# Performance work log

Hardware: AMD Instinct MI355X
Metric: run time of the kernel (lower is better)

Reference implementation:

```python
import jax, jax.numpy as jnp
import numpy as np

C_IN, C_OUT, K, H = 64, 128, 27, 100000

def setup_inputs() -> dict:
    key = jax.random.key(0)
    k1, k2, k3 = jax.random.split(key, 3)
    data_in = jax.random.normal(k1, (1, C_IN, H, 1), dtype=jnp.float32)
    # neighbor index table: 27 neighbors per node; -1 would mean 'missing' (zero-padded)
    neigh = jax.random.randint(k2, (H, K), 0, H, dtype=jnp.int64)
    # conv weight, fan-in scaled init, stored [C_out, C_in, K]
    weight = jax.random.normal(k3, (C_OUT, C_IN, K), dtype=jnp.float32) / np.sqrt(C_IN * K)
    return {"data_in": data_in, "neigh": neigh, "weight": weight}

def reference(data_in, neigh, weight):
    # data_in: [1, C_in, H, 1] (ocnn layout) -> [C_in, H]
    x = data_in[0, :, :, 0]
    # octree2col: gather 27 neighbors per node -> [C_in, H, K]
    cols = x[:, neigh]
    # zero out missing neighbors (index < 0)
    cols = jnp.where(neigh[None, :, :] >= 0, cols, jnp.zeros((), dtype=cols.dtype))
    # GEMM over (C_in, K) fused with ReLU -> [C_out, H]
    out = jnp.einsum('chk,ock->oh', cols, weight)
    out = jax.nn.relu(out)
    return out[None, :, :, None]  # back to ocnn layout [1, C_out, H, 1]
```

## Files before the change

### kernel.cpp

```cpp
#include <hip/hip_runtime.h>
#include <hip/hip_bf16.h>

#define C_IN  64
#define C_OUT 128
#define KK    27
#define HH    100000
#define TB    1563
#define WB    108
#define NBLK  391

typedef __attribute__((ext_vector_type(8))) short s8v;
typedef __attribute__((ext_vector_type(4))) float f32x4;
typedef __attribute__((ext_vector_type(4))) float f4v;
typedef __attribute__((ext_vector_type(4))) int   i4v;

__device__ inline unsigned short f2bf(float f) {
    __hip_bfloat16 h = __float2bfloat16(f);
    return *reinterpret_cast<unsigned short*>(&h);
}

__device__ inline void dma16(const void* g, void* l) {
    __builtin_amdgcn_global_load_lds((const __attribute__((address_space(1))) void*)g,
                                     (__attribute__((address_space(3))) void*)l, 16, 0, 0);
}

__global__ __launch_bounds__(256) void prep_kernel(const float* __restrict__ x,
                                                   const float* __restrict__ w,
                                                   unsigned short* __restrict__ xt,
                                                   unsigned short* __restrict__ wk) {
    const int tid = threadIdx.x;
    if (blockIdx.x < TB) {
        __shared__ __align__(16) unsigned short ts[64 * 72];
        const int hbase = blockIdx.x * 64;
        #pragma unroll
        for (int it = 0; it < 4; ++it) {
            int t = it * 256 + tid;
            int c = t >> 4, hg4 = t & 15;
            int hg = hbase + hg4 * 4;
            f4v v = (f4v){0.f, 0.f, 0.f, 0.f};
            if (hg < HH)
                v = __builtin_nontemporal_load((const f4v*)&x[(size_t)c * HH + hg]);
            ts[(hg4 * 4 + 0) * 72 + c] = f2bf(v.x);
            ts[(hg4 * 4 + 1) * 72 + c] = f2bf(v.y);
            ts[(hg4 * 4 + 2) * 72 + c] = f2bf(v.z);
            ts[(hg4 * 4 + 3) * 72 + c] = f2bf(v.w);
        }
        __syncthreads();
        #pragma unroll
        for (int it = 0; it < 2; ++it) {
            int u = it * 256 + tid;
            int hl = u >> 3, part = u & 7;
            int hg = hbase + hl;
            if (hg < HH)
                __builtin_nontemporal_store(*(const i4v*)&ts[hl * 72 + part * 8],
                                            (i4v*)&xt[(size_t)hg * 64 + part * 8]);
        }
    } else {
        int b = blockIdx.x - TB;
        if (b == 0 && tid < 64) {
            i4v z = (i4v){0, 0, 0, 0};
            *(i4v*)&xt[(size_t)HH * 64 + tid * 8] = z;
        }
        int base = b * 2048 + tid;
        #pragma unroll
        for (int j = 0; j < 8; ++j) {
            int t = base + j * 256;
            int jj = t & 63, o = (t >> 6) & 127, kx = t >> 13;
            int lc = (jj >> 3) ^ (o & 7);
            int c  = lc * 8 + (jj & 7);
            wk[t] = f2bf(w[(size_t)o * (C_IN * KK) + c * KK + kx]);
        }
    }
}

__global__ __launch_bounds__(256, 2) void conv_main(const unsigned short* __restrict__ xt,
                                                    const unsigned short* __restrict__ wk,
                                                    const int* __restrict__ neigh,
                                                    float* __restrict__ out) {
    __shared__ int neigh_s[256 * KK];
    __shared__ __align__(16) unsigned short w_s[2][128 * 64];

    const int tid  = threadIdx.x;
    const int wave = tid >> 6;
    const int lane = tid & 63;
    const int col  = lane & 15;
    const int quad = lane >> 4;
    const int hbase = blockIdx.x * 256;

    #pragma unroll
    for (int i = 0; i < 4; ++i) {
        int row_base = wave * 8 + i * 32;
        dma16(wk + row_base * 64 + lane * 8, &w_s[0][row_base * 64]);
    }

    int4 b0[2][4], b1[2][4];
    {
        #pragma unroll
        for (int nt = 0; nt < 4; ++nt) {
            int n  = wave * 64 + nt * 16 + col;
            int hg = hbase + n;
            int idx = (hg < HH) ? neigh[(size_t)hg * KK] : -1;
            int idxc = (idx < 0) ? HH : idx;
            const unsigned short* base = xt + (size_t)idxc * 64 + quad * 8;
            b0[0][nt] = *(const int4*)(base);
            b0[1][nt] = *(const int4*)(base + 32);
        }
    }

    #pragma unroll
    for (int j = 0; j < KK; ++j) {
        int i = j * 256 + tid;
        int hl = i / KK, kx = i - hl * KK;
        int hg = hbase + hl;
        neigh_s[i] = (hg < HH) ? __builtin_nontemporal_load(&neigh[(size_t)hg * KK + kx]) : -1;
    }

    f32x4 acc[8][4];
    #pragma unroll
    for (int mt = 0; mt < 8; ++mt)
        #pragma unroll
        for (int nt = 0; nt < 4; ++nt)
            acc[mt][nt] = (f32x4){0.f, 0.f, 0.f, 0.f};

    __syncthreads();

    auto loadB = [&](int kk, int4 (&frag)[2][4]) {
        #pragma unroll
        for (int nt = 0; nt < 4; ++nt) {
            int n = wave * 64 + nt * 16 + col;
            int idx = neigh_s[n * KK + kk];
            int idxc = (idx < 0) ? HH : idx;
            const unsigned short* base = xt + (size_t)idxc * 64 + quad * 8;
            frag[0][nt] = *(const int4*)(base);
            frag[1][nt] = *(const int4*)(base + 32);
        }
    };

    auto step = [&](int k, int4 (&cur)[2][4], int4 (&nxt)[2][4], bool last) {
        if (!last) {
            const unsigned short* src = wk + (size_t)(k + 1) * (C_OUT * C_IN);
            unsigned short* dst = &w_s[(k + 1) & 1][0];
            #pragma unroll
            for (int i = 0; i < 4; ++i) {
                int row_base = wave * 8 + i * 32;
                dma16(src + row_base * 64 + lane * 8, dst + row_base * 64);
            }
            loadB(k + 1, nxt);
        }

        const unsigned short* wp = &w_s[k & 1][0];
        #pragma unroll
        for (int ch = 0; ch < 2; ++ch) {
            const int pc = (ch * 4 + quad) ^ (col & 7);
            #pragma unroll
            for (int mt = 0; mt < 8; ++mt) {
                s8v a = *(const s8v*)&wp[(mt * 16 + col) * 64 + pc * 8];
                #pragma unroll
                for (int nt = 0; nt < 4; ++nt) {
                    s8v b = __builtin_bit_cast(s8v, cur[ch][nt]);
                    acc[mt][nt] = __builtin_amdgcn_mfma_f32_16x16x32_bf16(a, b, acc[mt][nt], 0, 0, 0);
                }
            }
        }

        if (!last) {
            asm volatile("s_waitcnt vmcnt(8) lgkmcnt(0)" ::: "memory");
            __builtin_amdgcn_s_barrier();
        }
    };

    #pragma unroll 1
    for (int k = 0; k < KK - 1; k += 2) {
        step(k,     b0, b1, false);
        step(k + 1, b1, b0, false);
    }
    step(KK - 1, b0, b1, true);

    #pragma unroll
    for (int mt = 0; mt < 8; ++mt) {
        #pragma unroll
        for (int nt = 0; nt < 4; ++nt) {
            int hg = hbase + wave * 64 + nt * 16 + col;
            if (hg < HH) {
                #pragma unroll
                for (int r = 0; r < 4; ++r) {
                    int o = mt * 16 + quad * 4 + r;
                    float v = acc[mt][nt][r];
                    v = v > 0.f ? v : 0.f;
                    __builtin_nontemporal_store(v, &out[(size_t)o * HH + hg]);
                }
            }
        }
    }
}

extern "C" void kernel_launch(void* const* d_in, const int* in_sizes, int n_in,
                              void* d_out, int out_size, void* d_ws, size_t ws_size,
                              hipStream_t stream) {
    const float* data_in = (const float*)d_in[0];
    const int*   neigh   = (const int*)d_in[1];
    const float* weight  = (const float*)d_in[2];
    float* out = (float*)d_out;

    unsigned short* xt = (unsigned short*)d_ws;
    unsigned short* wk = xt + (size_t)(HH + 8) * 64;

    prep_kernel<<<TB + WB, 256, 0, stream>>>(data_in, weight, xt, wk);
    conv_main<<<NBLK, 256, 0, stream>>>(xt, wk, neigh, out);
}
```

Measured before the change: 165.6 us.

## Triple-buffer weight DMA two steps ahead and batch transpose strips per block

The main conv kernel moves from double to triple buffering of the weight slices in LDS and issues each DMA two k-steps ahead. This lets the per-step wait drop its vmcnt requirement and keep only lgkmcnt(0). The prep kernel now processes 8 transpose strips per block, cutting its grid from 1563 to 196 blocks. Nontemporal hints are also removed from the neighbor loads and output stores. The extra LDS buffer raises shared memory use, which may reduce occupancy, and relying on barrier ordering without vmcnt for the gathered B fragments is a correctness risk.

```diff
diff --git a/kernel.cpp b/kernel.cpp
--- a/kernel.cpp
+++ b/kernel.cpp
@@ -5,7 +5,8 @@
 #define C_OUT 128
 #define KK    27
 #define HH    100000
-#define TB    1563
+#define TGB   196
+#define TSTRIPS 1563
 #define WB    108
 #define NBLK  391
 
@@ -29,34 +30,39 @@
                                                    unsigned short* __restrict__ xt,
                                                    unsigned short* __restrict__ wk) {
     const int tid = threadIdx.x;
-    if (blockIdx.x < TB) {
+    if (blockIdx.x < TGB) {
         __shared__ __align__(16) unsigned short ts[64 * 72];
-        const int hbase = blockIdx.x * 64;
-        #pragma unroll
-        for (int it = 0; it < 4; ++it) {
-            int t = it * 256 + tid;
-            int c = t >> 4, hg4 = t & 15;
-            int hg = hbase + hg4 * 4;
-            f4v v = (f4v){0.f, 0.f, 0.f, 0.f};
-            if (hg < HH)
-                v = __builtin_nontemporal_load((const f4v*)&x[(size_t)c * HH + hg]);
-            ts[(hg4 * 4 + 0) * 72 + c] = f2bf(v.x);
-            ts[(hg4 * 4 + 1) * 72 + c] = f2bf(v.y);
-            ts[(hg4 * 4 + 2) * 72 + c] = f2bf(v.z);
-            ts[(hg4 * 4 + 3) * 72 + c] = f2bf(v.w);
-        }
-        __syncthreads();
-        #pragma unroll
-        for (int it = 0; it < 2; ++it) {
-            int u = it * 256 + tid;
-            int hl = u >> 3, part = u & 7;
-            int hg = hbase + hl;
-            if (hg < HH)
-                __builtin_nontemporal_store(*(const i4v*)&ts[hl * 72 + part * 8],
-                                            (i4v*)&xt[(size_t)hg * 64 + part * 8]);
+        for (int s = 0; s < 8; ++s) {
+            int strip = blockIdx.x * 8 + s;
+            if (strip >= TSTRIPS) break;
+            const int hbase = strip * 64;
+            #pragma unroll
+            for (int it = 0; it < 4; ++it) {
+                int t = it * 256 + tid;
+                int c = t >> 4, hg4 = t & 15;
+                int hg = hbase + hg4 * 4;
+                f4v v = (f4v){0.f, 0.f, 0.f, 0.f};
+                if (hg < HH)
+                    v = __builtin_nontemporal_load((const f4v*)&x[(size_t)c * HH + hg]);
+                ts[(hg4 * 4 + 0) * 72 + c] = f2bf(v.x);
+                ts[(hg4 * 4 + 1) * 72 + c] = f2bf(v.y);
+                ts[(hg4 * 4 + 2) * 72 + c] = f2bf(v.z);
+                ts[(hg4 * 4 + 3) * 72 + c] = f2bf(v.w);
+            }
+            __syncthreads();
+            #pragma unroll
+            for (int it = 0; it < 2; ++it) {
+                int u = it * 256 + tid;
+                int hl = u >> 3, part = u & 7;
+                int hg = hbase + hl;
+                if (hg < HH)
+                    __builtin_nontemporal_store(*(const i4v*)&ts[hl * 72 + part * 8],
+                                                (i4v*)&xt[(size_t)hg * 64 + part * 8]);
+            }
+            __syncthreads();
         }
     } else {
-        int b = blockIdx.x - TB;
+        int b = blockIdx.x - TGB;
         if (b == 0 && tid < 64) {
             i4v z = (i4v){0, 0, 0, 0};
             *(i4v*)&xt[(size_t)HH * 64 + tid * 8] = z;
@@ -78,7 +84,7 @@
                                                     const int* __restrict__ neigh,
                                                     float* __restrict__ out) {
     __shared__ int neigh_s[256 * KK];
-    __shared__ __align__(16) unsigned short w_s[2][128 * 64];
+    __shared__ __align__(16) unsigned short w_s[3 * 128 * 64];
 
     const int tid  = threadIdx.x;
     const int wave = tid >> 6;
@@ -90,7 +96,7 @@
     #pragma unroll
     for (int i = 0; i < 4; ++i) {
         int row_base = wave * 8 + i * 32;
-        dma16(wk + row_base * 64 + lane * 8, &w_s[0][row_base * 64]);
+        dma16(wk + row_base * 64 + lane * 8, &w_s[0 * 8192 + row_base * 64]);
     }
 
     int4 b0[2][4], b1[2][4];
@@ -112,7 +118,14 @@
         int i = j * 256 + tid;
         int hl = i / KK, kx = i - hl * KK;
         int hg = hbase + hl;
-        neigh_s[i] = (hg < HH) ? __builtin_nontemporal_load(&neigh[(size_t)hg * KK + kx]) : -1;
+        neigh_s[i] = (hg < HH) ? neigh[(size_t)hg * KK + kx] : -1;
+    }
+
+    #pragma unroll
+    for (int i = 0; i < 4; ++i) {
+        int row_base = wave * 8 + i * 32;
+        dma16(wk + (size_t)1 * (C_OUT * C_IN) + row_base * 64 + lane * 8,
+              &w_s[1 * 8192 + row_base * 64]);
     }
 
     f32x4 acc[8][4];
@@ -136,19 +149,24 @@
         }
     };
 
-    auto step = [&](int k, int4 (&cur)[2][4], int4 (&nxt)[2][4], bool last) {
-        if (!last) {
-            const unsigned short* src = wk + (size_t)(k + 1) * (C_OUT * C_IN);
-            unsigned short* dst = &w_s[(k + 1) & 1][0];
+    int wc = 0;
+
+    auto step = [&](int k, int4 (&cur)[2][4], int4 (&nxt)[2][4], bool dma_far, bool do_next) {
+        if (dma_far) {
+            int wc2 = wc + 2; if (wc2 >= 3) wc2 -= 3;
+            const unsigned short* src = wk + (size_t)(k + 2) * (C_OUT * C_IN);
+            unsigned short* dst = &w_s[wc2 * 8192];
             #pragma unroll
             for (int i = 0; i < 4; ++i) {
                 int row_base = wave * 8 + i * 32;
                 dma16(src + row_base * 64 + lane * 8, dst + row_base * 64);
             }
+            __builtin_amdgcn_sched_barrier(0);
+        }
+        if (do_next)
             loadB(k + 1, nxt);
-        }
-
-        const unsigned short* wp = &w_s[k & 1][0];
+
+        const unsigned short* wp = &w_s[wc * 8192];
         #pragma unroll
         for (int ch = 0; ch < 2; ++ch) {
             const int pc = (ch * 4 + quad) ^ (col & 7);
@@ -163,18 +181,21 @@
             }
         }
 
-        if (!last) {
-            asm volatile("s_waitcnt vmcnt(8) lgkmcnt(0)" ::: "memory");
+        if (do_next) {
+            asm volatile("s_waitcnt lgkmcnt(0)" ::: "memory");
             __builtin_amdgcn_s_barrier();
         }
+        ++wc; if (wc == 3) wc = 0;
     };
 
     #pragma unroll 1
-    for (int k = 0; k < KK - 1; k += 2) {
-        step(k,     b0, b1, false);
-        step(k + 1, b1, b0, false);
-    }
-    step(KK - 1, b0, b1, true);
+    for (int k = 0; k < 24; k += 2) {
+        step(k,     b0, b1, true, true);
+        step(k + 1, b1, b0, true, true);
+    }
+    step(24, b0, b1, true,  true);
+    step(25, b1, b0, false, true);
+    step(26, b0, b1, false, false);
 
     #pragma unroll
     for (int mt = 0; mt < 8; ++mt) {
@@ -186,8 +207,7 @@
                 for (int r = 0; r < 4; ++r) {
                     int o = mt * 16 + quad * 4 + r;
                     float v = acc[mt][nt][r];
-                    v = v > 0.f ? v : 0.f;
-                    __builtin_nontemporal_store(v, &out[(size_t)o * HH + hg]);
+                    out[(size_t)o * HH + hg] = v > 0.f ? v : 0.f;
                 }
             }
         }
@@ -205,6 +225,6 @@
     unsigned short* xt = (unsigned short*)d_ws;
     unsigned short* wk = xt + (size_t)(HH + 8) * 64;
 
-    prep_kernel<<<TB + WB, 256, 0, stream>>>(data_in, weight, xt, wk);
+    prep_kernel<<<TGB + WB, 256, 0, stream>>>(data_in, weight, xt, wk);
     conv_main<<<NBLK, 256, 0, stream>>>(xt, wk, neigh, out);
 }
```

Measured after the change: 165.7 us. About the same (+0.0%).

## Split bf16 activations into two channel halves and triple-buffer weight slices

Applied to the files above, without the earlier changes.

Stores the transposed bf16 activation table as two separate 32-channel halves, so each gather fetches a 64-byte row instead of a 128-byte one. The K loop runs over 54 half-slices with a three-deep LDS weight ring that prefetches two slices ahead. The aim is a smaller random-gather footprint per step, better cache locality per half, and more overlap of weight DMA with compute. The cost is twice as many barrier-synchronised steps, two passes over the neighbour indices, and dropped nontemporal hints on stores and loads.

```diff
diff --git a/kernel.cpp b/kernel.cpp
--- a/kernel.cpp
+++ b/kernel.cpp
@@ -8,6 +8,9 @@
 #define TB    1563
 #define WB    108
 #define NBLK  391
+#define NSLICE (2 * KK)
+#define XTROW 32
+#define XTSZ  ((HH + 8) * XTROW)
 
 typedef __attribute__((ext_vector_type(8))) short s8v;
 typedef __attribute__((ext_vector_type(4))) float f32x4;
@@ -29,6 +32,8 @@
                                                    unsigned short* __restrict__ xt,
                                                    unsigned short* __restrict__ wk) {
     const int tid = threadIdx.x;
+    unsigned short* xt0 = xt;
+    unsigned short* xt1 = xt + XTSZ;
     if (blockIdx.x < TB) {
         __shared__ __align__(16) unsigned short ts[64 * 72];
         const int hbase = blockIdx.x * 64;
@@ -51,24 +56,32 @@
             int u = it * 256 + tid;
             int hl = u >> 3, part = u & 7;
             int hg = hbase + hl;
-            if (hg < HH)
-                __builtin_nontemporal_store(*(const i4v*)&ts[hl * 72 + part * 8],
-                                            (i4v*)&xt[(size_t)hg * 64 + part * 8]);
+            if (hg < HH) {
+                unsigned short* dst = (part < 4)
+                    ? &xt0[(size_t)hg * XTROW + part * 8]
+                    : &xt1[(size_t)hg * XTROW + (part - 4) * 8];
+                *(i4v*)dst = *(const i4v*)&ts[hl * 72 + part * 8];
+            }
         }
     } else {
         int b = blockIdx.x - TB;
-        if (b == 0 && tid < 64) {
+        if (b == 0 && tid < 8) {
+            unsigned short* base = (tid < 4) ? xt0 : xt1;
             i4v z = (i4v){0, 0, 0, 0};
-            *(i4v*)&xt[(size_t)HH * 64 + tid * 8] = z;
+            *(i4v*)&base[(size_t)HH * XTROW + (tid & 3) * 8] = z;
         }
         int base = b * 2048 + tid;
         #pragma unroll
         for (int j = 0; j < 8; ++j) {
             int t = base + j * 256;
-            int jj = t & 63, o = (t >> 6) & 127, kx = t >> 13;
-            int lc = (jj >> 3) ^ (o & 7);
-            int c  = lc * 8 + (jj & 7);
-            wk[t] = f2bf(w[(size_t)o * (C_IN * KK) + c * KK + kx]);
+            int half = t >= 110592;
+            int rem  = t - half * 110592;
+            int k  = rem >> 12;
+            int o  = (rem >> 5) & 127;
+            int jj = rem & 31;
+            int lc = (jj >> 3) ^ (o & 3);
+            int c  = half * 32 + lc * 8 + (jj & 7);
+            wk[t] = f2bf(w[(size_t)o * (C_IN * KK) + c * KK + k]);
         }
     }
 }
@@ -78,7 +91,7 @@
                                                     const int* __restrict__ neigh,
                                                     float* __restrict__ out) {
     __shared__ int neigh_s[256 * KK];
-    __shared__ __align__(16) unsigned short w_s[2][128 * 64];
+    __shared__ __align__(16) unsigned short w_s[3 * 128 * XTROW];
 
     const int tid  = threadIdx.x;
     const int wave = tid >> 6;
@@ -86,25 +99,22 @@
     const int col  = lane & 15;
     const int quad = lane >> 4;
     const int hbase = blockIdx.x * 256;
-
-    #pragma unroll
-    for (int i = 0; i < 4; ++i) {
-        int row_base = wave * 8 + i * 32;
-        dma16(wk + row_base * 64 + lane * 8, &w_s[0][row_base * 64]);
-    }
-
-    int4 b0[2][4], b1[2][4];
-    {
-        #pragma unroll
-        for (int nt = 0; nt < 4; ++nt) {
-            int n  = wave * 64 + nt * 16 + col;
-            int hg = hbase + n;
-            int idx = (hg < HH) ? neigh[(size_t)hg * KK] : -1;
-            int idxc = (idx < 0) ? HH : idx;
-            const unsigned short* base = xt + (size_t)idxc * 64 + quad * 8;
-            b0[0][nt] = *(const int4*)(base);
-            b0[1][nt] = *(const int4*)(base + 32);
-        }
+    const unsigned short* xh[2] = { xt, xt + XTSZ };
+
+    #pragma unroll
+    for (int i = 0; i < 2; ++i) {
+        int row_base = wave * 16 + i * 64;
+        dma16(wk + row_base * XTROW + lane * 8, &w_s[0 * 4096 + row_base * XTROW]);
+    }
+
+    int4 b0[4], b1[4];
+    #pragma unroll
+    for (int nt = 0; nt < 4; ++nt) {
+        int n  = wave * 64 + nt * 16 + col;
+        int hg = hbase + n;
+        int idx = (hg < HH) ? neigh[(size_t)hg * KK] : -1;
+        int idxc = (idx < 0) ? HH : idx;
+        b0[nt] = *(const int4*)(xh[0] + (size_t)idxc * XTROW + quad * 8);
     }
 
     #pragma unroll
@@ -112,7 +122,14 @@
         int i = j * 256 + tid;
         int hl = i / KK, kx = i - hl * KK;
         int hg = hbase + hl;
-        neigh_s[i] = (hg < HH) ? __builtin_nontemporal_load(&neigh[(size_t)hg * KK + kx]) : -1;
+        neigh_s[i] = (hg < HH) ? neigh[(size_t)hg * KK + kx] : -1;
+    }
+
+    #pragma unroll
+    for (int i = 0; i < 2; ++i) {
+        int row_base = wave * 16 + i * 64;
+        dma16(wk + (size_t)1 * (128 * XTROW) + row_base * XTROW + lane * 8,
+              &w_s[1 * 4096 + row_base * XTROW]);
     }
 
     f32x4 acc[8][4];
@@ -124,57 +141,62 @@
 
     __syncthreads();
 
-    auto loadB = [&](int kk, int4 (&frag)[2][4]) {
+    auto loadB = [&](int s, int4 (&frag)[4]) {
+        int half = s >= KK;
+        int kk = s - (half ? KK : 0);
+        const unsigned short* xb = xh[half];
         #pragma unroll
         for (int nt = 0; nt < 4; ++nt) {
             int n = wave * 64 + nt * 16 + col;
             int idx = neigh_s[n * KK + kk];
             int idxc = (idx < 0) ? HH : idx;
-            const unsigned short* base = xt + (size_t)idxc * 64 + quad * 8;
-            frag[0][nt] = *(const int4*)(base);
-            frag[1][nt] = *(const int4*)(base + 32);
+            frag[nt] = *(const int4*)(xb + (size_t)idxc * XTROW + quad * 8);
         }
     };
 
-    auto step = [&](int k, int4 (&cur)[2][4], int4 (&nxt)[2][4], bool last) {
-        if (!last) {
-            const unsigned short* src = wk + (size_t)(k + 1) * (C_OUT * C_IN);
-            unsigned short* dst = &w_s[(k + 1) & 1][0];
+    int wc = 0;
+
+    auto step = [&](int s, int4 (&cur)[4], int4 (&nxt)[4], bool dma_far, bool do_next) {
+        if (dma_far) {
+            int wc2 = wc + 2; if (wc2 >= 3) wc2 -= 3;
+            const unsigned short* src = wk + (size_t)(s + 2) * (128 * XTROW);
+            unsigned short* dst = &w_s[wc2 * 4096];
             #pragma unroll
-            for (int i = 0; i < 4; ++i) {
-                int row_base = wave * 8 + i * 32;
-                dma16(src + row_base * 64 + lane * 8, dst + row_base * 64);
-            }
-            loadB(k + 1, nxt);
-        }
-
-        const unsigned short* wp = &w_s[k & 1][0];
-        #pragma unroll
-        for (int ch = 0; ch < 2; ++ch) {
-            const int pc = (ch * 4 + quad) ^ (col & 7);
+            for (int i = 0; i < 2; ++i) {
+                int row_base = wave * 16 + i * 64;
+                dma16(src + row_base * XTROW + lane * 8, dst + row_base * XTROW);
+            }
+            __builtin_amdgcn_sched_barrier(0);
+        }
+        if (do_next)
+            loadB(s + 1, nxt);
+
+        const unsigned short* wp = &w_s[wc * 4096];
+        #pragma unroll
+        for (int mt = 0; mt < 8; ++mt) {
+            const int pc = quad ^ (col & 3);
+            s8v a = *(const s8v*)&wp[(mt * 16 + col) * XTROW + pc * 8];
             #pragma unroll
-            for (int mt = 0; mt < 8; ++mt) {
-                s8v a = *(const s8v*)&wp[(mt * 16 + col) * 64 + pc * 8];
-                #pragma unroll
-                for (int nt = 0; nt < 4; ++nt) {
-                    s8v b = __builtin_bit_cast(s8v, cur[ch][nt]);
-                    acc[mt][nt] = __builtin_amdgcn_mfma_f32_16x16x32_bf16(a, b, acc[mt][nt], 0, 0, 0);
-                }
-            }
-        }
-
-        if (!last) {
-            asm volatile("s_waitcnt vmcnt(8) lgkmcnt(0)" ::: "memory");
+            for (int nt = 0; nt < 4; ++nt) {
+                s8v b = __builtin_bit_cast(s8v, cur[nt]);
+                acc[mt][nt] = __builtin_amdgcn_mfma_f32_16x16x32_bf16(a, b, acc[mt][nt], 0, 0, 0);
+            }
+        }
+
+        if (do_next) {
+            asm volatile("s_waitcnt lgkmcnt(0)" ::: "memory");
             __builtin_amdgcn_s_barrier();
         }
+        ++wc; if (wc == 3) wc = 0;
     };
 
     #pragma unroll 1
-    for (int k = 0; k < KK - 1; k += 2) {
-        step(k,     b0, b1, false);
-        step(k + 1, b1, b0, false);
-    }
-    step(KK - 1, b0, b1, true);
+    for (int s = 0; s < NSLICE - 2; s += 2) {
+        step(s,     b0, b1, true, true);
+        step(s + 1, b1, b0, true, true);
+    }
+    step(NSLICE - 2, b0, b1, false, true);
+    step(NSLICE - 1, b1, b0, false, false);
 
     #pragma unroll
     for (int mt = 0; mt < 8; ++mt) {
@@ -186,8 +208,7 @@
                 for (int r = 0; r < 4; ++r) {
                     int o = mt * 16 + quad * 4 + r;
                     float v = acc[mt][nt][r];
-                    v = v > 0.f ? v : 0.f;
-                    __builtin_nontemporal_store(v, &out[(size_t)o * HH + hg]);
+                    out[(size_t)o * HH + hg] = v > 0.f ? v : 0.f;
                 }
             }
         }
@@ -203,7 +224,7 @@
     float* out = (float*)d_out;
 
     unsigned short* xt = (unsigned short*)d_ws;
-    unsigned short* wk = xt + (size_t)(HH + 8) * 64;
+    unsigned short* wk = xt + (size_t)2 * XTSZ;
 
     prep_kernel<<<TB + WB, 256, 0, stream>>>(data_in, weight, xt, wk);
     conv_main<<<NBLK, 256, 0, stream>>>(xt, wk, neigh, out);
```

Result: faster. 155.1 us (median of 2 runs) (-6.4%).
